# Optimization experiments

Hardware: AMD Instinct MI355X
Metric: run time of the kernel (lower is better)

The kernel has to match this reference:

```python
import jax, jax.numpy as jnp
import numpy as np

B, T, C = 8, 4096, 1024
NH = 64          # module sets self.n_head = dim_head = 64
HD = C // NH     # 16


def setup_inputs() -> dict:
    key = jax.random.key(0)
    ks = jax.random.split(key, 9)
    s = 1.0 / np.sqrt(C).astype(np.float32)
    x = jax.random.normal(ks[0], (B, T, C), jnp.float32)
    Wq = jax.random.normal(ks[1], (C, C), jnp.float32) * s
    bq = jax.random.normal(ks[2], (C,), jnp.float32) * 0.01
    Wk = jax.random.normal(ks[3], (C, C), jnp.float32) * s
    bk = jax.random.normal(ks[4], (C,), jnp.float32) * 0.01
    Wv = jax.random.normal(ks[5], (C, C), jnp.float32) * s
    bv = jax.random.normal(ks[6], (C,), jnp.float32) * 0.01
    Wp = jax.random.normal(ks[7], (C, C), jnp.float32) * s
    bp = jax.random.normal(ks[8], (C,), jnp.float32) * 0.01
    return {"x": x, "Wq": Wq, "bq": bq, "Wk": Wk, "bk": bk,
            "Wv": Wv, "bv": bv, "Wp": Wp, "bp": bp}


def _heads(t):
    # [B, T, C] -> [B, NH, T, HD]
    return t.reshape(B, T, NH, HD).transpose(0, 2, 1, 3)


def reference(x, Wq, bq, Wk, bk, Wv, bv, Wp, bp):
    # self-attention path: y = x; kv_mask=None (masked path is unreachable in source)
    q = _heads(x @ Wq.T + bq)
    k = _heads(x @ Wk.T + bk)
    v = _heads(x @ Wv.T + bv)
    q = jax.nn.softmax(q, axis=-1)
    k = jax.nn.softmax(k, axis=-1)
    k_cumsum = k.sum(axis=2, keepdims=True)               # [B, NH, 1, HD]
    D_inv = 1.0 / (q * k_cumsum).sum(axis=-1, keepdims=True)  # [B, NH, T, 1]
    context = jnp.einsum('bhtd,bhte->bhde', k, v)          # [B, NH, HD, HD]
    y = jnp.einsum('bhtd,bhde->bhte', q, context) * D_inv  # [B, NH, T, HD]
    y = y.transpose(0, 2, 1, 3).reshape(B, T, C)           # b h n d -> b n (h d)
    return y @ Wp.T + bp
```

## Files before the change

kernel.cpp:

```cpp
#include <hip/hip_runtime.h>
#include <stdint.h>


typedef __attribute__((ext_vector_type(8))) __bf16 bf16x8;
typedef __attribute__((ext_vector_type(4))) float f32x4;
typedef __attribute__((ext_vector_type(4))) unsigned int u32x4;
typedef __attribute__((ext_vector_type(4))) unsigned short u16x4;

#define AS1 __attribute__((address_space(1)))
#define AS3 __attribute__((address_space(3)))

__device__ __forceinline__ unsigned short f2bf(float f) {
  unsigned int u = __builtin_bit_cast(unsigned int, f);
  u += 0x7FFFu + ((u >> 16) & 1u);
  return (unsigned short)(u >> 16);
}

__device__ __forceinline__ void gl_lds16(const unsigned short* g, unsigned short* l) {
  __builtin_amdgcn_global_load_lds((const AS1 unsigned int*)g, (AS3 unsigned int*)l, 16, 0, 0);
}

__global__ __launch_bounds__(256)
void cvt_x(const float* __restrict__ src, unsigned short* __restrict__ dst, int n4) {
  int i = blockIdx.x * blockDim.x + threadIdx.x;
  const int stride = gridDim.x * blockDim.x;
  for (; i < n4; i += stride) {
    f32x4 v = *(const f32x4*)(src + (size_t)i * 4);
    u16x4 o;
    o.x = f2bf(v.x); o.y = f2bf(v.y); o.z = f2bf(v.z); o.w = f2bf(v.w);
    *(u16x4*)(dst + (size_t)i * 4) = o;
  }
}

__global__ __launch_bounds__(256)
void cvt_w(const float* __restrict__ w0, const float* __restrict__ w1,
           const float* __restrict__ w2, const float* __restrict__ w3,
           unsigned short* __restrict__ dst) {
  const int g = blockIdx.x * 256 + threadIdx.x;
  const int w = g >> 17;
  const int r = g & 131071;
  const int f = r >> 6;
  const int l = r & 63;
  const int n = (f >> 5) * 16 + (l & 15);
  const int k = (f & 31) * 32 + (l >> 4) * 8;
  const float* ws[4] = {w0, w1, w2, w3};
  const float* src = ws[w] + (size_t)n * 1024 + k;
  f32x4 v0 = *(const f32x4*)src;
  f32x4 v1 = *(const f32x4*)(src + 4);
  u16x4 a, b;
  a.x = f2bf(v0.x); a.y = f2bf(v0.y); a.z = f2bf(v0.z); a.w = f2bf(v0.w);
  b.x = f2bf(v1.x); b.y = f2bf(v1.y); b.z = f2bf(v1.z); b.w = f2bf(v1.w);
  unsigned short* o = dst + (size_t)g * 8;
  *(u16x4*)o = a;
  *(u16x4*)(o + 4) = b;
}

template<int KIND>
__global__ __launch_bounds__(256, 3)
void gemm_pipe(const unsigned short* __restrict__ A,
               const unsigned short* __restrict__ Wf,
               const float* __restrict__ b0, const float* __restrict__ b1,
               const float* __restrict__ b2,
               unsigned short* __restrict__ oq, unsigned short* __restrict__ okT,
               unsigned short* __restrict__ ovT, float* __restrict__ of)
{
  __shared__ __align__(16) unsigned short lds[12288];

  const int tid  = threadIdx.x;
  const int lane = tid & 63;
  const int wid  = tid >> 6;

  const int flat  = blockIdx.x;
  const int xcd   = flat & 7;
  const int i     = flat >> 3;
  const int bcg   = i >> 8;
  const int r     = i & 255;
  const int panel = r >> 3;
  const int c     = r & 7;
  const int brow  = (xcd * 32 + panel) * 128;
  const int bcol  = (bcg * 8 + c) * 128;

  const int srow = wid * 16 + (lane >> 2);
  const int scol = ((lane & 3) ^ ((lane >> 3) & 3)) << 3;
  const unsigned short* a_src = A + (size_t)(brow + srow) * 1024 + scol;
  unsigned short* Ldst = lds + wid * 512;

  const int wm = (wid >> 1) * 64;
  const int wn = (wid & 1) * 64;
  const int fr = lane & 15;
  const int fg = lane >> 4;
  const int aoff = (wm + fr) * 32 + ((fg ^ ((fr >> 1) & 3)) << 3);

  const unsigned short* wfp = Wf + ((size_t)((bcol + wn) >> 4) * 32) * 512 + lane * 8;

  const f32x4 fz = {0.f, 0.f, 0.f, 0.f};
  f32x4 acc[4][4];
  #pragma unroll
  for (int mt = 0; mt < 4; ++mt)
    #pragma unroll
    for (int nt = 0; nt < 4; ++nt) acc[mt][nt] = fz;

  auto stage = [&](int t, int buf) {
    unsigned short* d = Ldst + buf * 4096;
    gl_lds16(a_src + t * 32, d);
    gl_lds16(a_src + t * 32 + 65536, d + 2048);
  };
  auto loadB = [&](int t, bf16x8 (&dst)[4]) {
    #pragma unroll
    for (int nt = 0; nt < 4; ++nt)
      dst[nt] = __builtin_bit_cast(bf16x8,
        *(const u32x4*)(wfp + (size_t)t * 512 + (size_t)nt * 16384));
  };

  bf16x8 brgA[4], brgB[4];

  loadB(0, brgA);
  stage(0, 0); stage(1, 1); stage(2, 2);
  asm volatile("s_waitcnt vmcnt(4)" ::: "memory");
  __builtin_amdgcn_sched_barrier(0);
  __builtin_amdgcn_s_barrier();

  auto body = [&](int t, bf16x8 (&bc)[4], bf16x8 (&bn)[4]) {
    const unsigned short* Lb = lds + (t % 3) * 4096;
    bf16x8 af[4];
    #pragma unroll
    for (int mt = 0; mt < 4; ++mt)
      af[mt] = __builtin_bit_cast(bf16x8, *(const u32x4*)&Lb[aoff + mt * 512]);
    asm volatile("s_waitcnt lgkmcnt(0)" ::: "memory");
    __builtin_amdgcn_sched_barrier(0);
    __builtin_amdgcn_s_barrier();
    if (t + 3 < 32) stage(t + 3, t % 3);
    if (t + 1 < 32) loadB(t + 1, bn);
    if (t <= 28)      asm volatile("s_waitcnt vmcnt(6)" ::: "memory");
    else if (t <= 30) asm volatile("s_waitcnt vmcnt(4)" ::: "memory");
    else              asm volatile("s_waitcnt vmcnt(0)" ::: "memory");
    __builtin_amdgcn_sched_barrier(0);
    __builtin_amdgcn_s_setprio(1);
    #pragma unroll
    for (int mt = 0; mt < 4; ++mt)
      #pragma unroll
      for (int nt = 0; nt < 4; ++nt)
        acc[mt][nt] = __builtin_amdgcn_mfma_f32_16x16x32_bf16(af[mt], bc[nt], acc[mt][nt], 0, 0, 0);
    __builtin_amdgcn_s_setprio(0);
    __builtin_amdgcn_s_barrier();
  };

  for (int t = 0; t < 32; t += 2) {
    body(t,     brgA, brgB);
    body(t + 1, brgB, brgA);
  }

  const int sec = (KIND == 0) ? (bcol >> 10) : 0;
  const float* bias = (KIND == 1) ? b0 : (sec == 0 ? b0 : (sec == 1 ? b1 : b2));

  #pragma unroll
  for (int nt = 0; nt < 4; ++nt) {
    const int n_glob = bcol + wn + nt * 16 + fr;
    const int nn = (KIND == 0) ? (n_glob & 1023) : n_glob;
    const float bv = bias[nn];
    #pragma unroll
    for (int mt = 0; mt < 4; ++mt) {
      const int m0 = brow + wm + mt * 16 + fg * 4;
      float vals[4];
      #pragma unroll
      for (int r2 = 0; r2 < 4; ++r2) vals[r2] = acc[mt][nt][r2] + bv;

      if (KIND == 0 && sec <= 1) {
        #pragma unroll
        for (int r2 = 0; r2 < 4; ++r2) {
          float x = vals[r2];
          float mx = x;
          #pragma unroll
          for (int s = 1; s < 16; s <<= 1) mx = fmaxf(mx, __shfl_xor(mx, s, 64));
          float e = __expf(x - mx);
          float sm = e;
          #pragma unroll
          for (int s = 1; s < 16; s <<= 1) sm += __shfl_xor(sm, s, 64);
          vals[r2] = e / sm;
        }
      }

      if (KIND == 1) {
        #pragma unroll
        for (int r2 = 0; r2 < 4; ++r2)
          of[(size_t)(m0 + r2) * 1024 + n_glob] = vals[r2];
      } else if (sec == 0) {
        #pragma unroll
        for (int r2 = 0; r2 < 4; ++r2)
          oq[(size_t)(m0 + r2) * 1024 + nn] = f2bf(vals[r2]);
      } else {
        unsigned short* o = (sec == 1) ? okT : ovT;
        const int bb = m0 >> 12;
        const int t0 = m0 & 4095;
        const int hh = nn >> 4;
        const int dd = nn & 15;
        u16x4 pk;
        pk.x = f2bf(vals[0]); pk.y = f2bf(vals[1]);
        pk.z = f2bf(vals[2]); pk.w = f2bf(vals[3]);
        *(u16x4*)&o[(((size_t)bb * 64 + hh) * 16 + dd) * 4096 + t0] = pk;
      }
    }
  }
}

__global__ __launch_bounds__(256)
void attn_kernel(const unsigned short* __restrict__ qb,
                 const unsigned short* __restrict__ kT,
                 const unsigned short* __restrict__ vT,
                 unsigned short* __restrict__ yb)
{
  const int head = blockIdx.x;
  const int tid  = threadIdx.x;
  const int lane = tid & 63;
  const int wid  = tid >> 6;
  const int fr   = lane & 15;
  const int fg   = lane >> 4;

  const unsigned short* kTh = kT + (size_t)head * 16 * 4096;
  const unsigned short* vTh = vT + (size_t)head * 16 * 4096;

  const u32x4 uz = {0u, 0u, 0u, 0u};
  const f32x4 fz = {0.f, 0.f, 0.f, 0.f};
  const u32x4 uo = {0x3F803F80u, 0x3F803F80u, 0x3F803F80u, 0x3F803F80u};
  const bf16x8 ones = __builtin_bit_cast(bf16x8, uo);

  f32x4 cctx = fz, ckc = fz;
  #pragma unroll 4
  for (int t0 = wid * 1024; t0 < (wid + 1) * 1024; t0 += 32) {
    bf16x8 ak = __builtin_bit_cast(bf16x8, *(const u32x4*)&kTh[(size_t)fr * 4096 + t0 + fg * 8]);
    bf16x8 bv = __builtin_bit_cast(bf16x8, *(const u32x4*)&vTh[(size_t)fr * 4096 + t0 + fg * 8]);
    cctx = __builtin_amdgcn_mfma_f32_16x16x32_bf16(ak, bv, cctx, 0, 0, 0);
    ckc  = __builtin_amdgcn_mfma_f32_16x16x32_bf16(ak, ones, ckc, 0, 0, 0);
  }

  __shared__ float red[4][16][16];
  __shared__ float kcr[4][16];
  __shared__ float ctxf[16][16];
  __shared__ float kcf[16];

  #pragma unroll
  for (int r = 0; r < 4; ++r) red[wid][fg * 4 + r][fr] = cctx[r];
  if (fr == 0) {
    #pragma unroll
    for (int r = 0; r < 4; ++r) kcr[wid][fg * 4 + r] = ckc[r];
  }
  __syncthreads();
  {
    const int d = tid >> 4, e = tid & 15;
    ctxf[d][e] = red[0][d][e] + red[1][d][e] + red[2][d][e] + red[3][d][e];
    if (tid < 16) kcf[tid] = kcr[0][tid] + kcr[1][tid] + kcr[2][tid] + kcr[3][tid];
  }
  __syncthreads();

  bf16x8 bctx = __builtin_bit_cast(bf16x8, uz);
  bf16x8 bkc  = __builtin_bit_cast(bf16x8, uz);
  if (fg < 2) {
    #pragma unroll
    for (int j = 0; j < 8; ++j) {
      const int d = fg * 8 + j;
      bctx[j] = (__bf16)ctxf[d][fr];
      bkc[j]  = (__bf16)kcf[d];
    }
  }

  const int b = head >> 6;
  const int h = head & 63;
  const size_t qbase = (size_t)b * 4096 * 1024 + (size_t)h * 16;

  for (int step = 0; step < 64; ++step) {
    const int t0 = step * 64 + wid * 16;
    bf16x8 af = __builtin_bit_cast(bf16x8, uz);
    if (fg < 2)
      af = __builtin_bit_cast(bf16x8, *(const u32x4*)&qb[qbase + (size_t)(t0 + fr) * 1024 + fg * 8]);
    f32x4 cy = __builtin_amdgcn_mfma_f32_16x16x32_bf16(af, bctx, fz, 0, 0, 0);
    f32x4 cd = __builtin_amdgcn_mfma_f32_16x16x32_bf16(af, bkc,  fz, 0, 0, 0);
    #pragma unroll
    for (int r = 0; r < 4; ++r) {
      const int t = t0 + fg * 4 + r;
      const float yv = cy[r] * __builtin_amdgcn_rcpf(cd[r]);
      yb[qbase + (size_t)t * 1024 + fr] = f2bf(yv);
    }
  }
}

extern "C" void kernel_launch(void* const* d_in, const int* in_sizes, int n_in,
                              void* d_out, int out_size, void* d_ws, size_t ws_size,
                              hipStream_t stream)
{
  (void)in_sizes; (void)n_in; (void)out_size; (void)ws_size;
  const float* x  = (const float*)d_in[0];
  const float* Wq = (const float*)d_in[1];
  const float* bq = (const float*)d_in[2];
  const float* Wk = (const float*)d_in[3];
  const float* bk = (const float*)d_in[4];
  const float* Wv = (const float*)d_in[5];
  const float* bv = (const float*)d_in[6];
  const float* Wp = (const float*)d_in[7];
  const float* bp = (const float*)d_in[8];

  char* ws = (char*)d_ws;
  unsigned short* xb  = (unsigned short*)(ws);
  unsigned short* wb  = (unsigned short*)(ws + 67108864);
  unsigned short* qb  = (unsigned short*)(ws + 75497472);
  unsigned short* kTb = (unsigned short*)(ws + 142606336);
  unsigned short* vTb = (unsigned short*)(ws + 209715200);

  cvt_x<<<2048, 256, 0, stream>>>(x, xb, 33554432 / 4);
  cvt_w<<<2048, 256, 0, stream>>>(Wq, Wk, Wv, Wp, wb);

  gemm_pipe<0><<<6144, 256, 0, stream>>>(xb, wb, bq, bk, bv, qb, kTb, vTb, nullptr);

  attn_kernel<<<512, 256, 0, stream>>>(qb, kTb, vTb, xb );

  gemm_pipe<1><<<2048, 256, 0, stream>>>(xb , wb + 3145728, bp, bp, bp,
                                         nullptr, nullptr, nullptr, (float*)d_out);
}
```

Before: 507.8 us.

## Replace 128x128 GEMM with 256x256-tile, 8-wave double-buffered GEMM

Swaps the 128x128 triple-buffered GEMM for a 256x256 tile run by 512 threads in 8 waves, each computing 128x64 with K steps of 64. Loads of A into LDS and B into registers are interleaved between the four MFMA groups, and blocks are remapped to XCDs for the new grid. Larger tiles raise arithmetic intensity and cut global traffic. The cost is more registers and LDS per block, fewer blocks in flight, and a full vmcnt(0) wait each iteration that may expose latency.

Result: slower. 561.8 us (+10.6%).

```diff
diff --git a/kernel.cpp b/kernel.cpp
--- a/kernel.cpp
+++ b/kernel.cpp
@@ -55,115 +55,127 @@
   *(u16x4*)(o + 4) = b;
 }
 
+
+#define MFMA16(Q, BR) do {                                                   \
+  __builtin_amdgcn_s_setprio(1);                                             \
+  _Pragma("unroll")                                                          \
+  for (int mi = 0; mi < 8; ++mi) {                                           \
+    acc[mi][Q] = __builtin_amdgcn_mfma_f32_16x16x32_bf16(aF[mi][0], BR[0], acc[mi][Q], 0, 0, 0); \
+    acc[mi][Q] = __builtin_amdgcn_mfma_f32_16x16x32_bf16(aF[mi][1], BR[1], acc[mi][Q], 0, 0, 0); \
+  }                                                                          \
+  __builtin_amdgcn_s_setprio(0);                                             \
+} while (0)
+
 template<int KIND>
-__global__ __launch_bounds__(256, 3)
-void gemm_pipe(const unsigned short* __restrict__ A,
-               const unsigned short* __restrict__ Wf,
-               const float* __restrict__ b0, const float* __restrict__ b1,
-               const float* __restrict__ b2,
-               unsigned short* __restrict__ oq, unsigned short* __restrict__ okT,
-               unsigned short* __restrict__ ovT, float* __restrict__ of)
+__global__ __launch_bounds__(512, 2)
+void gemm256(const unsigned short* __restrict__ A,
+             const unsigned short* __restrict__ Wf,
+             const float* __restrict__ b0, const float* __restrict__ b1,
+             const float* __restrict__ b2,
+             unsigned short* __restrict__ oq, unsigned short* __restrict__ okT,
+             unsigned short* __restrict__ ovT, float* __restrict__ of)
 {
-  __shared__ __align__(16) unsigned short lds[12288];
+  __shared__ __align__(16) unsigned short lds[32768];
 
   const int tid  = threadIdx.x;
   const int lane = tid & 63;
   const int wid  = tid >> 6;
-
-  const int flat  = blockIdx.x;
-  const int xcd   = flat & 7;
-  const int i     = flat >> 3;
-  const int bcg   = i >> 8;
-  const int r     = i & 255;
-  const int panel = r >> 3;
-  const int c     = r & 7;
-  const int brow  = (xcd * 32 + panel) * 128;
-  const int bcol  = (bcg * 8 + c) * 128;
-
-  const int srow = wid * 16 + (lane >> 2);
-  const int scol = ((lane & 3) ^ ((lane >> 3) & 3)) << 3;
-  const unsigned short* a_src = A + (size_t)(brow + srow) * 1024 + scol;
-  unsigned short* Ldst = lds + wid * 512;
-
-  const int wm = (wid >> 1) * 64;
-  const int wn = (wid & 1) * 64;
-  const int fr = lane & 15;
-  const int fg = lane >> 4;
-  const int aoff = (wm + fr) * 32 + ((fg ^ ((fr >> 1) & 3)) << 3);
-
-  const unsigned short* wfp = Wf + ((size_t)((bcol + wn) >> 4) * 32) * 512 + lane * 8;
+  const int wm   = wid >> 2;
+  const int wn   = wid & 3;
+  const int fr   = lane & 15;
+  const int fg   = lane >> 4;
+
+  const int flat = blockIdx.x;
+  const int xcd  = flat & 7;
+  const int vid  = flat >> 3;
+  int brow_t, bcol_t;
+  if (KIND == 0) {
+    const int cg = vid / 48, r1 = vid % 48;
+    const int pg = r1 / 12, r2 = r1 % 12;
+    brow_t = xcd * 16 + pg * 4 + r2 / 3;
+    bcol_t = cg * 3 + r2 % 3;
+  } else {
+    const int pg = vid >> 4, r1 = vid & 15;
+    brow_t = xcd * 16 + pg * 4 + (r1 >> 2);
+    bcol_t = r1 & 3;
+  }
+  const int brow = brow_t * 256;
+  const int bcol = bcol_t * 256;
+
+  const int scol = (((lane & 7) ^ ((lane >> 3) & 7)) << 3);
+  const unsigned short* a_src = A + (size_t)(brow + wid * 32 + (lane >> 3)) * 1024 + scol;
+  unsigned short* a_dst = lds + wid * 2048 + (lane & 0) ;
+
+  auto stA = [&](int kt, int buf, int s) {
+    gl_lds16(a_src + (size_t)s * 8192 + kt * 64,
+             lds + buf * 16384 + (wid * 4 + s) * 512);
+  };
+
+  const char* aP = (const char*)lds + (size_t)(wm * 128 + fr) * 128;
+  const int sl0 = ((fg ^ (fr & 7)) << 4);
+  const int sl1 = (((4 | fg) ^ (fr & 7)) << 4);
+
+  const unsigned short* wfp = Wf + (size_t)((bcol + wn * 64) >> 4) * 32 * 512 + lane * 8;
+  auto loadB = [&](int kt, int ni, bf16x8 (&d)[2]) {
+    d[0] = __builtin_bit_cast(bf16x8, *(const u32x4*)(wfp + (size_t)(ni * 32 + kt * 2) * 512));
+    d[1] = __builtin_bit_cast(bf16x8, *(const u32x4*)(wfp + (size_t)(ni * 32 + kt * 2 + 1) * 512));
+  };
 
   const f32x4 fz = {0.f, 0.f, 0.f, 0.f};
-  f32x4 acc[4][4];
+  f32x4 acc[8][4];
   #pragma unroll
-  for (int mt = 0; mt < 4; ++mt)
-    #pragma unroll
-    for (int nt = 0; nt < 4; ++nt) acc[mt][nt] = fz;
-
-  auto stage = [&](int t, int buf) {
-    unsigned short* d = Ldst + buf * 4096;
-    gl_lds16(a_src + t * 32, d);
-    gl_lds16(a_src + t * 32 + 65536, d + 2048);
-  };
-  auto loadB = [&](int t, bf16x8 (&dst)[4]) {
-    #pragma unroll
-    for (int nt = 0; nt < 4; ++nt)
-      dst[nt] = __builtin_bit_cast(bf16x8,
-        *(const u32x4*)(wfp + (size_t)t * 512 + (size_t)nt * 16384));
-  };
-
-  bf16x8 brgA[4], brgB[4];
-
-  loadB(0, brgA);
-  stage(0, 0); stage(1, 1); stage(2, 2);
-  asm volatile("s_waitcnt vmcnt(4)" ::: "memory");
-  __builtin_amdgcn_sched_barrier(0);
-  __builtin_amdgcn_s_barrier();
-
-  auto body = [&](int t, bf16x8 (&bc)[4], bf16x8 (&bn)[4]) {
-    const unsigned short* Lb = lds + (t % 3) * 4096;
-    bf16x8 af[4];
-    #pragma unroll
-    for (int mt = 0; mt < 4; ++mt)
-      af[mt] = __builtin_bit_cast(bf16x8, *(const u32x4*)&Lb[aoff + mt * 512]);
-    asm volatile("s_waitcnt lgkmcnt(0)" ::: "memory");
+  for (int mi = 0; mi < 8; ++mi)
+    #pragma unroll
+    for (int ni = 0; ni < 4; ++ni) acc[mi][ni] = fz;
+
+  bf16x8 aF[8][2];
+  bf16x8 bEven[2], bOdd[2];
+
+  stA(0, 0, 0); stA(0, 0, 1); stA(0, 0, 2); stA(0, 0, 3);
+  loadB(0, 0, bEven);
+
+  for (int t = 0; t < 16; ++t) {
+    const bool nl = (t < 15);
+    const int nb = (t + 1) & 1;
+    const int bufB = (t & 1) * 32768;
+
+    asm volatile("s_waitcnt vmcnt(0)" ::: "memory");
     __builtin_amdgcn_sched_barrier(0);
     __builtin_amdgcn_s_barrier();
-    if (t + 3 < 32) stage(t + 3, t % 3);
-    if (t + 1 < 32) loadB(t + 1, bn);
-    if (t <= 28)      asm volatile("s_waitcnt vmcnt(6)" ::: "memory");
-    else if (t <= 30) asm volatile("s_waitcnt vmcnt(4)" ::: "memory");
-    else              asm volatile("s_waitcnt vmcnt(0)" ::: "memory");
     __builtin_amdgcn_sched_barrier(0);
-    __builtin_amdgcn_s_setprio(1);
-    #pragma unroll
-    for (int mt = 0; mt < 4; ++mt)
-      #pragma unroll
-      for (int nt = 0; nt < 4; ++nt)
-        acc[mt][nt] = __builtin_amdgcn_mfma_f32_16x16x32_bf16(af[mt], bc[nt], acc[mt][nt], 0, 0, 0);
-    __builtin_amdgcn_s_setprio(0);
-    __builtin_amdgcn_s_barrier();
-  };
-
-  for (int t = 0; t < 32; t += 2) {
-    body(t,     brgA, brgB);
-    body(t + 1, brgB, brgA);
+
+    if (nl) stA(t + 1, nb, 0);
+    loadB(t, 1, bOdd);
+    #pragma unroll
+    for (int mi = 0; mi < 8; ++mi) {
+      aF[mi][0] = __builtin_bit_cast(bf16x8, *(const u32x4*)(aP + bufB + mi * 2048 + sl0));
+      aF[mi][1] = __builtin_bit_cast(bf16x8, *(const u32x4*)(aP + bufB + mi * 2048 + sl1));
+    }
+    MFMA16(0, bEven);
+    if (nl) stA(t + 1, nb, 1);
+    loadB(t, 2, bEven);
+    MFMA16(1, bOdd);
+    if (nl) stA(t + 1, nb, 2);
+    loadB(t, 3, bOdd);
+    MFMA16(2, bEven);
+    if (nl) { stA(t + 1, nb, 3); loadB(t + 1, 0, bEven); }
+    MFMA16(3, bOdd);
   }
 
   const int sec = (KIND == 0) ? (bcol >> 10) : 0;
   const float* bias = (KIND == 1) ? b0 : (sec == 0 ? b0 : (sec == 1 ? b1 : b2));
 
   #pragma unroll
-  for (int nt = 0; nt < 4; ++nt) {
-    const int n_glob = bcol + wn + nt * 16 + fr;
+  for (int ni = 0; ni < 4; ++ni) {
+    const int n_glob = bcol + wn * 64 + ni * 16 + fr;
     const int nn = (KIND == 0) ? (n_glob & 1023) : n_glob;
     const float bv = bias[nn];
     #pragma unroll
-    for (int mt = 0; mt < 4; ++mt) {
-      const int m0 = brow + wm + mt * 16 + fg * 4;
+    for (int mi = 0; mi < 8; ++mi) {
+      const int m0 = brow + wm * 128 + mi * 16 + fg * 4;
       float vals[4];
       #pragma unroll
-      for (int r2 = 0; r2 < 4; ++r2) vals[r2] = acc[mt][nt][r2] + bv;
+      for (int r2 = 0; r2 < 4; ++r2) vals[r2] = acc[mi][ni][r2] + bv;
 
       if (KIND == 0 && sec <= 1) {
         #pragma unroll
@@ -308,10 +320,10 @@
   cvt_x<<<2048, 256, 0, stream>>>(x, xb, 33554432 / 4);
   cvt_w<<<2048, 256, 0, stream>>>(Wq, Wk, Wv, Wp, wb);
 
-  gemm_pipe<0><<<6144, 256, 0, stream>>>(xb, wb, bq, bk, bv, qb, kTb, vTb, nullptr);
+  gemm256<0><<<1536, 512, 0, stream>>>(xb, wb, bq, bk, bv, qb, kTb, vTb, nullptr);
 
   attn_kernel<<<512, 256, 0, stream>>>(qb, kTb, vTb, xb );
 
-  gemm_pipe<1><<<2048, 256, 0, stream>>>(xb , wb + 3145728, bp, bp, bp,
-                                         nullptr, nullptr, nullptr, (float*)d_out);
-}
+  gemm256<1><<<512, 512, 0, stream>>>(xb , wb + 3145728, bp, bp, bp,
+                                      nullptr, nullptr, nullptr, (float*)d_out);
+}
```
